# Kernel tuning notes

Measured on AMD Instinct MI355X. Metric: run time of the kernel, lower is better.

## Reference

```python
import jax, jax.numpy as jnp
import numpy as np

N = 40000      # nodes
E = 640000     # edges
G = 64         # graphs in batch
F_IN = 128
H = 128


def setup_inputs() -> dict:
    key = jax.random.key(0)
    ks = jax.random.split(key, 10)
    x = jax.random.normal(ks[0], (N, F_IN), dtype=jnp.float32)
    edge_index = jax.random.randint(ks[1], (2, E), 0, N, dtype=jnp.int64)
    batch = jnp.sort(jax.random.randint(ks[2], (N,), 0, G, dtype=jnp.int64))
    s = 0.05
    W1 = jax.random.normal(ks[3], (F_IN, H), dtype=jnp.float32) * s
    W2 = jax.random.normal(ks[4], (H, H), dtype=jnp.float32) * s
    W3 = jax.random.normal(ks[5], (H, H), dtype=jnp.float32) * s
    Wl = jax.random.normal(ks[6], (H, 1), dtype=jnp.float32) * s
    b1 = jnp.zeros((H,), jnp.float32)
    b2 = jnp.zeros((H,), jnp.float32)
    b3 = jnp.zeros((H,), jnp.float32)
    bl = jnp.zeros((1,), jnp.float32)
    return {"x": x, "edge_index": edge_index, "batch": batch, "dropout_rate": 0,
            "W1": W1, "b1": b1, "W2": W2, "b2": b2, "W3": W3, "b3": b3,
            "Wl": Wl, "bl": bl}


def _gcn_norm(edge_index, n):
    # PyG GCNConv default: add self-loops, symmetric deg^{-1/2} normalization.
    loop = jnp.arange(n, dtype=edge_index.dtype)
    row = jnp.concatenate([edge_index[0], loop])  # source
    col = jnp.concatenate([edge_index[1], loop])  # target
    ones = jnp.ones(row.shape[0], jnp.float32)
    deg = jax.ops.segment_sum(ones, col, num_segments=n)
    dis = jnp.where(deg > 0, jax.lax.rsqrt(deg), 0.0)
    norm = dis[row] * dis[col]  # [E+N]
    return row, col, norm


def _gcn_conv(x, row, col, norm, W, b, n):
    h = x @ W + b                       # dense transform [N,H]
    msg = h[row] * norm[:, None]        # gather + scale  [E+N,H]
    return jax.ops.segment_sum(msg, col, num_segments=n)


def reference(x, edge_index, batch, dropout_rate, W1, b1, W2, b2, W3, b3, Wl, bl):
    n = x.shape[0]
    row, col, norm = _gcn_norm(edge_index, n)
    # eval mode: dropout(p=dropout_rate, training=False) is identity
    h = jax.nn.relu(_gcn_conv(x, row, col, norm, W1, b1, n))
    h = jax.nn.relu(_gcn_conv(h, row, col, norm, W2, b2, n))
    h = jax.nn.relu(_gcn_conv(h, row, col, norm, W3, b3, n))
    # global mean pool over graphs
    sums = jax.ops.segment_sum(h, batch, num_segments=G)           # [G,H]
    cnt = jax.ops.segment_sum(jnp.ones(n, jnp.float32), batch, num_segments=G)
    pooled = sums / jnp.maximum(cnt, 1.0)[:, None]
    return pooled @ Wl + bl             # [G,1]
```

## Files before the change

### kernel.cpp

```cpp
#include <hip/hip_runtime.h>

constexpr int N = 40000;
constexpr int E = 640000;
constexpr int G = 64;
constexpr int H = 128;

constexpr int NB      = (N + 255) / 256;
constexpr int EB      = (E + 255) / 256;
constexpr int GEMM1_B = N / 64;
constexpr int FUSED_B = N / 32;
constexpr int POOL_B  = N / 32;
constexpr int NXCD    = 8;

constexpr int CAP     = 64;
constexpr int QPN     = CAP / 4;
constexpr int CSRE    = N * CAP + 8;

typedef float    floatx2 __attribute__((ext_vector_type(2)));
typedef float    f32x4   __attribute__((ext_vector_type(4)));
typedef _Float16 f16x8   __attribute__((ext_vector_type(8)));

__device__ __forceinline__ unsigned pack_fp8x4(float a, float b, float c, float d) {
    unsigned v = 0;
    v = __builtin_amdgcn_cvt_pk_fp8_f32(a, b, v, false);
    v = __builtin_amdgcn_cvt_pk_fp8_f32(c, d, v, true);
    return v;
}

__device__ __forceinline__ void pk_fma(floatx2& acc, floatx2 a, floatx2 w2) {
    asm("v_pk_fma_f32 %0, %1, %2, %0" : "+v"(acc) : "v"(a), "v"(w2));
}

__device__ __forceinline__ void fma8p(floatx2& aclo, floatx2& achi, unsigned r, float w) {
    floatx2 lo = __builtin_amdgcn_cvt_pk_f32_fp8(r, false);
    floatx2 hi = __builtin_amdgcn_cvt_pk_f32_fp8(r, true);
    floatx2 w2 = {w, w};
    pk_fma(aclo, lo, w2);
    pk_fma(achi, hi, w2);
}

__device__ __forceinline__ float entry_w(int e) {
    floatx2 hi = __builtin_amdgcn_cvt_pk_f32_fp8((unsigned)e, true);
    return hi.y;
}
__device__ __forceinline__ int entry_src(int e) { return e & 0xFFFFFF; }

__device__ __forceinline__ f16x8 cvt8(float4 a, float4 b) {
    f16x8 r;
    r[0] = (_Float16)a.x; r[1] = (_Float16)a.y; r[2] = (_Float16)a.z; r[3] = (_Float16)a.w;
    r[4] = (_Float16)b.x; r[5] = (_Float16)b.y; r[6] = (_Float16)b.z; r[7] = (_Float16)b.w;
    return r;
}

__device__ __forceinline__ float4 aggregate_node(const unsigned* __restrict__ h8,
                                                 const int4* __restrict__ csr4,
                                                 const int* __restrict__ deg,
                                                 const float* __restrict__ dis,
                                                 int i, int c) {
    float d = dis[i];
    floatx2 aclo = {0.f, 0.f}, achi = {0.f, 0.f};
    fma8p(aclo, achi, h8[(size_t)i * 32 + c], d * d);
    int cq = deg[i]; cq = (cq > CAP) ? CAP : cq;
    int p  = i * QPN;
    int p1 = p + (((cq + 7) & ~7) >> 2);
    for (; p < p1; p += 2) {
        int4 ea = csr4[p], eb = csr4[p + 1];
        unsigned r0 = h8[(size_t)entry_src(ea.x) * 32 + c];
        unsigned r1 = h8[(size_t)entry_src(ea.y) * 32 + c];
        unsigned r2 = h8[(size_t)entry_src(ea.z) * 32 + c];
        unsigned r3 = h8[(size_t)entry_src(ea.w) * 32 + c];
        unsigned r4 = h8[(size_t)entry_src(eb.x) * 32 + c];
        unsigned r5 = h8[(size_t)entry_src(eb.y) * 32 + c];
        unsigned r6 = h8[(size_t)entry_src(eb.z) * 32 + c];
        unsigned r7 = h8[(size_t)entry_src(eb.w) * 32 + c];
        fma8p(aclo, achi, r0, entry_w(ea.x)); fma8p(aclo, achi, r1, entry_w(ea.y));
        fma8p(aclo, achi, r2, entry_w(ea.z)); fma8p(aclo, achi, r3, entry_w(ea.w));
        fma8p(aclo, achi, r4, entry_w(eb.x)); fma8p(aclo, achi, r5, entry_w(eb.y));
        fma8p(aclo, achi, r6, entry_w(eb.z)); fma8p(aclo, achi, r7, entry_w(eb.w));
    }
    return make_float4(aclo.x, aclo.y, achi.x, achi.y);
}

__global__ void prep_wt1(const float* __restrict__ W1, _Float16* __restrict__ wt) {
    const int g  = blockIdx.x * 256 + threadIdx.x;
    const int f  = g >> 4;
    const int k0 = (g & 15) * 8;
    f16x8 v;
    #pragma unroll
    for (int j = 0; j < 8; ++j) v[j] = (_Float16)W1[(size_t)(k0 + j) * H + f];
    *reinterpret_cast<f16x8*>(wt + f * H + k0) = v;
}

__global__ __launch_bounds__(256) void gemm1_and_count8(const float* __restrict__ X,
                                                        const _Float16* __restrict__ wt1,
                                                        const float* __restrict__ b,
                                                        unsigned* __restrict__ Y,
                                                        const int* __restrict__ col,
                                                        int* __restrict__ cnt8,
                                                        const float* __restrict__ W2,
                                                        const float* __restrict__ W3,
                                                        _Float16* __restrict__ wt) {
    __shared__ uint4 WTl[2048];
    const int blk = blockIdx.x;
    const int tid = threadIdx.x;
    if (blk >= GEMM1_B + EB) {
        const int pb = blk - (GEMM1_B + EB);
        const int m  = 1 + (pb >> 3);
        const float* W = (m == 1) ? W2 : W3;
        const int g  = (pb & 7) * 256 + tid;
        const int f  = g >> 4;
        const int k0 = (g & 15) * 8;
        f16x8 v;
        #pragma unroll
        for (int j = 0; j < 8; ++j) v[j] = (_Float16)W[(size_t)(k0 + j) * H + f];
        *reinterpret_cast<f16x8*>(wt + ((size_t)m << 14) + f * H + k0) = v;
        return;
    }
    if (blk >= GEMM1_B) {
        int e = (blk - GEMM1_B) * 256 + tid;
        if (e < E) {
            int r = (e >> 8) & 7;
            atomicAdd(&cnt8[r * N + col[e]], 1);
        }
        return;
    }
    const uint4* wtg = reinterpret_cast<const uint4*>(wt1);
    #pragma unroll
    for (int i = 0; i < 8; ++i) {
        int g = i * 256 + tid;
        WTl[g ^ ((g >> 4) & 7)] = wtg[g];
    }
    __syncthreads();

    const int lane = tid & 63;
    const int wv   = tid >> 6;
    const int c    = lane & 15;
    const int grp  = lane >> 4;
    const int node = blk * 64 + wv * 16 + c;

    const f32x4* b4 = reinterpret_cast<const f32x4*>(b);
    f32x4 acc[8];
    #pragma unroll
    for (int mt = 0; mt < 8; ++mt) acc[mt] = b4[mt * 4 + grp];

    const float4* X4 = reinterpret_cast<const float4*>(X);
    #pragma unroll
    for (int ks = 0; ks < 4; ++ks) {
        const int k0 = ks * 32 + grp * 8;
        float4 xa = X4[(size_t)node * 32 + (k0 >> 2)];
        float4 xb = X4[(size_t)node * 32 + (k0 >> 2) + 1];
        f16x8 bfr = cvt8(xa, xb);
        #pragma unroll
        for (int mt = 0; mt < 8; ++mt) {
            const int f = mt * 16 + c;
            const int g = (f << 4) + (k0 >> 3);
            f16x8 afr = *reinterpret_cast<const f16x8*>(&WTl[g ^ (f & 7)]);
            acc[mt] = __builtin_amdgcn_mfma_f32_16x16x32_f16(afr, bfr, acc[mt], 0, 0, 0);
        }
    }
    #pragma unroll
    for (int mt = 0; mt < 8; ++mt) {
        const int jg = mt * 4 + grp;
        Y[(size_t)node * 32 + jg] = pack_fp8x4(acc[mt][0], acc[mt][1], acc[mt][2], acc[mt][3]);
    }
}

__global__ void mid_deg_dis(int* __restrict__ cnt8, int* __restrict__ deg,
                            float* __restrict__ dis) {
    int i = blockIdx.x * 256 + threadIdx.x;
    if (i >= N) return;
    int base = 0;
    #pragma unroll
    for (int r = 0; r < NXCD; ++r) {
        int v = cnt8[r * N + i];
        cnt8[r * N + i] = base;
        base += v;
    }
    deg[i] = base;
    dis[i] = rsqrtf((float)(base + 1));
}

__global__ __launch_bounds__(256) void fill_stamped(const int* __restrict__ row,
                                                    const int* __restrict__ col,
                                                    const float* __restrict__ dis,
                                                    int* __restrict__ cnt8,
                                                    int* __restrict__ csr) {
    int e = blockIdx.x * 256 + threadIdx.x;
    if (e >= E) return;
    int rsrc = row[e], cdst = col[e];
    float w = dis[rsrc] * dis[cdst];
    unsigned wb = __builtin_amdgcn_cvt_pk_fp8_f32(w, 0.0f, 0, false) & 0xFFu;
    int r = (e >> 8) & 7;
    int p = atomicAdd(&cnt8[r * N + cdst], 1);
    if (p < CAP) csr[cdst * CAP + p] = (int)((wb << 24) | (unsigned)rsrc);
}

__global__ __launch_bounds__(256) void fused_agg_gemm(const unsigned* __restrict__ t_in,
                                                      const int4* __restrict__ csr4,
                                                      const int* __restrict__ deg,
                                                      const float* __restrict__ dis,
                                                      const _Float16* __restrict__ wt,
                                                      const float* __restrict__ b,
                                                      unsigned* __restrict__ t_out) {
    __shared__ float4 tile[32 * 32];
    const int tid = threadIdx.x;
    const int node0 = blockIdx.x * 32;

    {
        const int cc = tid & 31;
        const int nl = tid >> 5;
        #pragma unroll
        for (int sub = 0; sub < 4; ++sub) {
            const int local = sub * 8 + nl;
            float4 acc = aggregate_node(t_in, csr4, deg, dis, node0 + local, cc);
            acc.x = fmaxf(acc.x, 0.f); acc.y = fmaxf(acc.y, 0.f);
            acc.z = fmaxf(acc.z, 0.f); acc.w = fmaxf(acc.w, 0.f);
            tile[(local * 32 + cc) ^ (local & 7)] = acc;
        }
    }
    __syncthreads();

    const int lane = tid & 63;
    const int wv   = tid >> 6;
    const int c    = lane & 15;
    const int grp  = lane >> 4;

    const f32x4* b4 = reinterpret_cast<const f32x4*>(b);
    f32x4 acc00, acc01, acc10, acc11;
    acc00 = acc01 = b4[(2 * wv + 0) * 4 + grp];
    acc10 = acc11 = b4[(2 * wv + 1) * 4 + grp];

    const uint4* wtg = reinterpret_cast<const uint4*>(wt);
    #pragma unroll
    for (int ks = 0; ks < 4; ++ks) {
        const int k0 = ks * 32 + grp * 8;
        f16x8 bfr0, bfr1;
        {
            int nd = c;
            int g0 = nd * 32 + (k0 >> 2);
            float4 ta = tile[g0 ^ (nd & 7)];
            float4 tb = tile[(g0 + 1) ^ (nd & 7)];
            bfr0 = cvt8(ta, tb);
            nd = 16 + c;
            g0 = nd * 32 + (k0 >> 2);
            ta = tile[g0 ^ (nd & 7)];
            tb = tile[(g0 + 1) ^ (nd & 7)];
            bfr1 = cvt8(ta, tb);
        }
        {
            int f = (2 * wv + 0) * 16 + c;
            f16x8 afr = *reinterpret_cast<const f16x8*>(&wtg[f * 16 + (k0 >> 3)]);
            acc00 = __builtin_amdgcn_mfma_f32_16x16x32_f16(afr, bfr0, acc00, 0, 0, 0);
            acc01 = __builtin_amdgcn_mfma_f32_16x16x32_f16(afr, bfr1, acc01, 0, 0, 0);
            f = (2 * wv + 1) * 16 + c;
            afr = *reinterpret_cast<const f16x8*>(&wtg[f * 16 + (k0 >> 3)]);
            acc10 = __builtin_amdgcn_mfma_f32_16x16x32_f16(afr, bfr0, acc10, 0, 0, 0);
            acc11 = __builtin_amdgcn_mfma_f32_16x16x32_f16(afr, bfr1, acc11, 0, 0, 0);
        }
    }

    const int jg0 = (2 * wv + 0) * 4 + grp;
    const int jg1 = (2 * wv + 1) * 4 + grp;
    const int nA = node0 + c, nB = node0 + 16 + c;
    t_out[(size_t)nA * 32 + jg0] = pack_fp8x4(acc00[0], acc00[1], acc00[2], acc00[3]);
    t_out[(size_t)nB * 32 + jg0] = pack_fp8x4(acc01[0], acc01[1], acc01[2], acc01[3]);
    t_out[(size_t)nA * 32 + jg1] = pack_fp8x4(acc10[0], acc10[1], acc10[2], acc10[3]);
    t_out[(size_t)nB * 32 + jg1] = pack_fp8x4(acc11[0], acc11[1], acc11[2], acc11[3]);
}

__global__ __launch_bounds__(256) void agg_pool(const unsigned* __restrict__ t_in,
                                                const int4* __restrict__ csr4,
                                                const int* __restrict__ deg,
                                                const float* __restrict__ dis,
                                                const int* __restrict__ batch,
                                                float* __restrict__ pooled) {
    __shared__ float4 tile[32 * 32];
    const int tid = threadIdx.x;
    const int c  = tid & 31;
    const int nl = tid >> 5;
    const int i0 = blockIdx.x * 32;

    #pragma unroll
    for (int sub = 0; sub < 4; ++sub) {
        const int local = sub * 8 + nl;
        float4 acc = aggregate_node(t_in, csr4, deg, dis, i0 + local, c);
        acc.x = fmaxf(acc.x, 0.f); acc.y = fmaxf(acc.y, 0.f);
        acc.z = fmaxf(acc.z, 0.f); acc.w = fmaxf(acc.w, 0.f);
        tile[local * 32 + c] = acc;
    }
    __syncthreads();

    if (tid < 128) {
        const int j = tid;
        const float* tf = reinterpret_cast<const float*>(tile);
        int cur = batch[i0];
        float s = 0.0f;
        #pragma unroll
        for (int r = 0; r < 32; ++r) {
            int g = batch[i0 + r];
            if (g != cur) { atomicAdd(&pooled[cur * H + j], s); s = 0.0f; cur = g; }
            s += tf[r * 128 + j];
        }
        atomicAdd(&pooled[cur * H + j], s);
    }
}

__global__ __launch_bounds__(128) void head(const float* __restrict__ pooled,
                                            const int* __restrict__ batch,
                                            const float* __restrict__ Wl,
                                            const float* __restrict__ bl,
                                            float* __restrict__ out) {
    const int g = blockIdx.x;
    const int j = threadIdx.x;
    __shared__ int bounds[2];
    if (j < 2) {
        int target = g + j;
        int lo = 0, hi = N;
        while (lo < hi) {
            int mid = (lo + hi) >> 1;
            if (batch[mid] < target) lo = mid + 1; else hi = mid;
        }
        bounds[j] = lo;
    }
    __syncthreads();
    float cnt = fmaxf((float)(bounds[1] - bounds[0]), 1.0f);
    float val = (pooled[g * H + j] / cnt) * Wl[j];
    __shared__ float red[128];
    red[j] = val;
    __syncthreads();
    #pragma unroll
    for (int s = 64; s > 0; s >>= 1) {
        if (j < s) red[j] += red[j + s];
        __syncthreads();
    }
    if (j == 0) out[g] = red[0] + bl[0];
}

extern "C" void kernel_launch(void* const* d_in, const int* in_sizes, int n_in,
                              void* d_out, int out_size, void* d_ws, size_t ws_size,
                              hipStream_t stream) {
    const float* x     = (const float*)d_in[0];
    const int*   ei    = (const int*)  d_in[1];
    const int*   batch = (const int*)  d_in[2];
    const float* W1 = (const float*)d_in[4];
    const float* b1 = (const float*)d_in[5];
    const float* W2 = (const float*)d_in[6];
    const float* b2 = (const float*)d_in[7];
    const float* W3 = (const float*)d_in[8];
    const float* b3 = (const float*)d_in[9];
    const float* Wl = (const float*)d_in[10];
    const float* bl = (const float*)d_in[11];
    float* out = (float*)d_out;

    const int* row = ei;
    const int* col = ei + E;

    auto align256 = [](size_t v) { return (v + 255) & ~(size_t)255; };
    char* ws = (char*)d_ws;
    size_t off = 0;
    int*   cnt8   = (int*)(ws + off);
    float* pooled = (float*)(cnt8 + (size_t)NXCD * N);
    int*   csr    = (int*)(pooled + (size_t)G * H);
    size_t zero_bytes = (size_t)NXCD * N * 4 + (size_t)G * H * 4 + (size_t)CSRE * 4;
    off += align256(zero_bytes);
    float*    dis = (float*)(ws + off); off += align256((size_t)N * 4);
    int*      deg = (int*)  (ws + off); off += align256((size_t)N * 4);
    _Float16* wt  = (_Float16*)(ws + off); off += align256((size_t)3 * H * H * 2);
    unsigned* bufA = (unsigned*)(ws + off); off += align256((size_t)N * H);
    unsigned* bufB = (unsigned*)(ws + off); off += align256((size_t)N * H);
    (void)ws_size; (void)n_in; (void)in_sizes; (void)out_size;

    const int4* csr4 = reinterpret_cast<const int4*>(csr);
    _Float16* wt1 = wt;
    _Float16* wt2 = wt + (size_t)H * H;
    _Float16* wt3 = wt + (size_t)2 * H * H;

    (void)hipMemsetAsync(cnt8, 0, zero_bytes, stream);
    prep_wt1<<<8, 256, 0, stream>>>(W1, wt1);
    gemm1_and_count8<<<GEMM1_B + EB + 16, 256, 0, stream>>>(x, wt1, b1, bufA, col,
                                                            cnt8, W2, W3, wt);
    mid_deg_dis<<<NB, 256, 0, stream>>>(cnt8, deg, dis);
    fill_stamped<<<EB, 256, 0, stream>>>(row, col, dis, cnt8, csr);
    fused_agg_gemm<<<FUSED_B, 256, 0, stream>>>(bufA, csr4, deg, dis, wt2, b2, bufB);
    fused_agg_gemm<<<FUSED_B, 256, 0, stream>>>(bufB, csr4, deg, dis, wt3, b3, bufA);
    agg_pool<<<POOL_B, 256, 0, stream>>>(bufA, csr4, deg, dis, batch, pooled);
    head<<<G, 128, 0, stream>>>(pooled, batch, Wl, bl, out);
}
```

Measured before the change: 218.7 us.

## Fold W1 transpose into GEMM1 and fuse head into pooling via last-block ticket

```diff
diff --git a/kernel.cpp b/kernel.cpp
--- a/kernel.cpp
+++ b/kernel.cpp
@@ -81,18 +81,8 @@
     return make_float4(aclo.x, aclo.y, achi.x, achi.y);
 }
 
-__global__ void prep_wt1(const float* __restrict__ W1, _Float16* __restrict__ wt) {
-    const int g  = blockIdx.x * 256 + threadIdx.x;
-    const int f  = g >> 4;
-    const int k0 = (g & 15) * 8;
-    f16x8 v;
-    #pragma unroll
-    for (int j = 0; j < 8; ++j) v[j] = (_Float16)W1[(size_t)(k0 + j) * H + f];
-    *reinterpret_cast<f16x8*>(wt + f * H + k0) = v;
-}
-
 __global__ __launch_bounds__(256) void gemm1_and_count8(const float* __restrict__ X,
-                                                        const _Float16* __restrict__ wt1,
+                                                        const float* __restrict__ W1,
                                                         const float* __restrict__ b,
                                                         unsigned* __restrict__ Y,
                                                         const int* __restrict__ col,
@@ -124,11 +114,15 @@
         }
         return;
     }
-    const uint4* wtg = reinterpret_cast<const uint4*>(wt1);
     #pragma unroll
     for (int i = 0; i < 8; ++i) {
         int g = i * 256 + tid;
-        WTl[g ^ ((g >> 4) & 7)] = wtg[g];
+        const int f  = g >> 4;
+        const int k0 = (g & 15) * 8;
+        f16x8 v;
+        #pragma unroll
+        for (int j = 0; j < 8; ++j) v[j] = (_Float16)W1[(size_t)(k0 + j) * H + f];
+        *reinterpret_cast<f16x8*>(&WTl[g ^ (f & 7)]) = v;
     }
     __syncthreads();
 
@@ -268,12 +262,16 @@
     t_out[(size_t)nB * 32 + jg1] = pack_fp8x4(acc11[0], acc11[1], acc11[2], acc11[3]);
 }
 
-__global__ __launch_bounds__(256) void agg_pool(const unsigned* __restrict__ t_in,
-                                                const int4* __restrict__ csr4,
-                                                const int* __restrict__ deg,
-                                                const float* __restrict__ dis,
-                                                const int* __restrict__ batch,
-                                                float* __restrict__ pooled) {
+__global__ __launch_bounds__(256) void agg_pool_head(const unsigned* __restrict__ t_in,
+                                                     const int4* __restrict__ csr4,
+                                                     const int* __restrict__ deg,
+                                                     const float* __restrict__ dis,
+                                                     const int* __restrict__ batch,
+                                                     float* __restrict__ pooled,
+                                                     const float* __restrict__ Wl,
+                                                     const float* __restrict__ bl,
+                                                     float* __restrict__ out,
+                                                     int* __restrict__ donecnt) {
     __shared__ float4 tile[32 * 32];
     const int tid = threadIdx.x;
     const int c  = tid & 31;
@@ -303,37 +301,33 @@
         }
         atomicAdd(&pooled[cur * H + j], s);
     }
-}
-
-__global__ __launch_bounds__(128) void head(const float* __restrict__ pooled,
-                                            const int* __restrict__ batch,
-                                            const float* __restrict__ Wl,
-                                            const float* __restrict__ bl,
-                                            float* __restrict__ out) {
-    const int g = blockIdx.x;
-    const int j = threadIdx.x;
-    __shared__ int bounds[2];
-    if (j < 2) {
-        int target = g + j;
-        int lo = 0, hi = N;
-        while (lo < hi) {
-            int mid = (lo + hi) >> 1;
-            if (batch[mid] < target) lo = mid + 1; else hi = mid;
-        }
-        bounds[j] = lo;
-    }
-    __syncthreads();
-    float cnt = fmaxf((float)(bounds[1] - bounds[0]), 1.0f);
-    float val = (pooled[g * H + j] / cnt) * Wl[j];
-    __shared__ float red[128];
-    red[j] = val;
-    __syncthreads();
-    #pragma unroll
-    for (int s = 64; s > 0; s >>= 1) {
-        if (j < s) red[j] += red[j + s];
-        __syncthreads();
-    }
-    if (j == 0) out[g] = red[0] + bl[0];
+
+    __threadfence();
+    __shared__ int ticket_s;
+    __syncthreads();
+    if (tid == 0) ticket_s = atomicAdd(donecnt, 1);
+    __syncthreads();
+    if (ticket_s != POOL_B - 1) return;
+
+    const int w = tid >> 6;
+    const int l = tid & 63;
+    for (int g = w; g < G; g += 4) {
+        int target = g + (l & 1);
+        int a = 0, bnd = N;
+        while (a < bnd) {
+            int mid = (a + bnd) >> 1;
+            if (batch[mid] < target) a = mid + 1; else bnd = mid;
+        }
+        int lo = __shfl(a, 0);
+        int hi = __shfl(a, 1);
+        float cnt = fmaxf((float)(hi - lo), 1.0f);
+        float v0 = atomicAdd(&pooled[g * H + l], 0.0f)      * Wl[l];
+        float v1 = atomicAdd(&pooled[g * H + l + 64], 0.0f) * Wl[l + 64];
+        float s = (v0 + v1) / cnt;
+        #pragma unroll
+        for (int o = 32; o > 0; o >>= 1) s += __shfl_down(s, o);
+        if (l == 0) out[g] = s + bl[0];
+    }
 }
 
 extern "C" void kernel_launch(void* const* d_in, const int* in_sizes, int n_in,
@@ -358,10 +352,11 @@
     auto align256 = [](size_t v) { return (v + 255) & ~(size_t)255; };
     char* ws = (char*)d_ws;
     size_t off = 0;
-    int*   cnt8   = (int*)(ws + off);
-    float* pooled = (float*)(cnt8 + (size_t)NXCD * N);
-    int*   csr    = (int*)(pooled + (size_t)G * H);
-    size_t zero_bytes = (size_t)NXCD * N * 4 + (size_t)G * H * 4 + (size_t)CSRE * 4;
+    int*   cnt8    = (int*)(ws + off);
+    float* pooled  = (float*)(cnt8 + (size_t)NXCD * N);
+    int*   donecnt = (int*)(pooled + (size_t)G * H);
+    int*   csr     = donecnt + 4;
+    size_t zero_bytes = (size_t)NXCD * N * 4 + (size_t)G * H * 4 + 16 + (size_t)CSRE * 4;
     off += align256(zero_bytes);
     float*    dis = (float*)(ws + off); off += align256((size_t)N * 4);
     int*      deg = (int*)  (ws + off); off += align256((size_t)N * 4);
@@ -371,18 +366,16 @@
     (void)ws_size; (void)n_in; (void)in_sizes; (void)out_size;
 
     const int4* csr4 = reinterpret_cast<const int4*>(csr);
-    _Float16* wt1 = wt;
     _Float16* wt2 = wt + (size_t)H * H;
     _Float16* wt3 = wt + (size_t)2 * H * H;
 
     (void)hipMemsetAsync(cnt8, 0, zero_bytes, stream);
-    prep_wt1<<<8, 256, 0, stream>>>(W1, wt1);
-    gemm1_and_count8<<<GEMM1_B + EB + 16, 256, 0, stream>>>(x, wt1, b1, bufA, col,
+    gemm1_and_count8<<<GEMM1_B + EB + 16, 256, 0, stream>>>(x, W1, b1, bufA, col,
                                                             cnt8, W2, W3, wt);
     mid_deg_dis<<<NB, 256, 0, stream>>>(cnt8, deg, dis);
     fill_stamped<<<EB, 256, 0, stream>>>(row, col, dis, cnt8, csr);
     fused_agg_gemm<<<FUSED_B, 256, 0, stream>>>(bufA, csr4, deg, dis, wt2, b2, bufB);
     fused_agg_gemm<<<FUSED_B, 256, 0, stream>>>(bufB, csr4, deg, dis, wt3, b3, bufA);
-    agg_pool<<<POOL_B, 256, 0, stream>>>(bufA, csr4, deg, dis, batch, pooled);
-    head<<<G, 128, 0, stream>>>(pooled, batch, Wl, bl, out);
-}
+    agg_pool_head<<<POOL_B, 256, 0, stream>>>(bufA, csr4, deg, dis, batch, pooled,
+                                              Wl, bl, out, donecnt);
+}
```

Result: slower. 367.7 us (+68.1%).
